# Kernel optimization log

Hardware: AMD Instinct MI355X
Metric: run time of the kernel (lower is better)

The kernel has to match this reference:

```python
import jax, jax.numpy as jnp
import numpy as np

KEEP_RATIO = 0.25
BLOCK = 8
TEMP = 0.1


def setup_inputs() -> dict:
    key = jax.random.key(0)
    features = jax.random.normal(key, (8, 256, 132, 132), dtype=jnp.float32)
    return {"features": features, "enabled": 1}


def reference(features, enabled):
    B, C, H, W = features.shape
    if not enabled:
        return jnp.ones((B, C, H, W), dtype=features.dtype)
    # pad H, W up to multiples of BLOCK (zeros, like F.pad default)
    ph = (-H) % BLOCK
    pw = (-W) % BLOCK
    x = jnp.pad(jnp.abs(features), ((0, 0), (0, 0), (0, ph), (0, pw)))
    Hp, Wp = H + ph, W + pw
    nh, nw = Hp // BLOCK, Wp // BLOCK
    # avg_pool2d(kernel=stride=BLOCK) == block-mean via reshape
    pooled = x.reshape(B, C, nh, BLOCK, nw, BLOCK).mean(axis=(3, 5))  # [B,C,nh,nw]
    total = nh * nw
    scores = pooled.reshape(B, C, total)
    keep = max(1, min(total, int(round(total * KEEP_RATIO))))
    top_vals, top_idx = jax.lax.top_k(scores, keep)  # sorted descending, like torch.topk
    # hard mask: scatter ones at topk indices
    flat_idx = top_idx.reshape(B * C, keep)
    hard = (jnp.zeros((B * C, total), dtype=features.dtype)
            .at[jnp.arange(B * C)[:, None], flat_idx].set(1.0)
            .reshape(B, C, total))
    # training-mode straight-through soft blend
    thr = jax.lax.stop_gradient(top_vals[..., -1:])  # kth value as threshold
    soft = jax.nn.sigmoid((scores - thr) / TEMP)
    soft = soft * (keep / jnp.maximum(soft.sum(-1, keepdims=True), 1e-6))
    soft = jnp.clip(soft, 0.0, 1.0)
    mask = jax.lax.stop_gradient(hard) - jax.lax.stop_gradient(soft) + soft
    # upsample blocks back to pixels (repeat_interleave) and crop padding
    block_mask = mask.reshape(B, C, nh, nw)
    full = jnp.repeat(jnp.repeat(block_mask, BLOCK, axis=2), BLOCK, axis=3)
    return full[:, :, :H, :W]
```

## Files before the change

### kernel.cpp

```cpp
#include <hip/hip_runtime.h>


#define HH 132
#define WW 132
#define NB 17
#define TOTAL 289
#define KEEP 72
#define NTHREADS 256

__global__ __launch_bounds__(NTHREADS)
void gate_kernel(const float* __restrict__ feats,
                 const int* __restrict__ enabled_p,
                 float* __restrict__ out) {
    const int plane = blockIdx.x;
    const int t = threadIdx.x;
    const float* __restrict__ fp = feats + (size_t)plane * (HH * WW);
    float* __restrict__ op = out + (size_t)plane * (HH * WW);

    __shared__ double s_col[WW];
    __shared__ double s_score[TOTAL];
    __shared__ float  s_hard[TOTAL];

    for (int br = 0; br < NB; ++br) {
        const int r0 = br * 8;
        const int nr = (r0 + 8 <= HH) ? 8 : (HH - r0);
        if (t < WW) {
            double acc = 0.0;
            const float* rp = fp + (size_t)r0 * WW + t;
            #pragma unroll
            for (int k = 0; k < 8; ++k) {
                if (k < nr) acc += (double)fabsf(rp[k * WW]);
            }
            s_col[t] = acc;
        }
        __syncthreads();
        if (t < NB) {
            const int c0 = t * 8;
            const int nc = (c0 + 8 <= WW) ? 8 : (WW - c0);
            double s = 0.0;
            for (int j = 0; j < nc; ++j) s += s_col[c0 + j];
            s_score[br * NB + t] = s;
        }
        __syncthreads();
    }

    const int en = *enabled_p;
    for (int i = t; i < TOTAL; i += NTHREADS) {
        const double si = s_score[i];
        int rank = 0;
        for (int j = 0; j < TOTAL; ++j) {
            const double sj = s_score[j];
            rank += (int)((sj > si) || ((sj == si) && (j < i)));
        }
        s_hard[i] = (!en || rank < KEEP) ? 1.0f : 0.0f;
    }
    __syncthreads();

    constexpr int NV = (HH * WW) / 4;
    float4* __restrict__ op4 = (float4*)op;
    for (int v = t; v < NV; v += NTHREADS) {
        const int base = v * 4;
        const int row = base / WW;
        const int col = base - row * WW;
        const float m = s_hard[(row >> 3) * NB + (col >> 3)];
        op4[v] = make_float4(m, m, m, m);
    }
}

extern "C" void kernel_launch(void* const* d_in, const int* in_sizes, int n_in,
                              void* d_out, int out_size, void* d_ws, size_t ws_size,
                              hipStream_t stream) {
    const float* feats = (const float*)d_in[0];
    const int* enabled = (const int*)d_in[1];
    float* out = (float*)d_out;
    const int planes = 8 * 256;
    gate_kernel<<<planes, NTHREADS, 0, stream>>>(feats, enabled, out);
}
```

Before: 269.7 us.

## Compute block sums per thread with float4 loads, removing per-row-band syncs

Replaces the 17-iteration column-sum-then-reduce loop, which has two barriers per band, with one thread per 8x8 block. Each thread reads its block with float4 loads and accumulates in two double accumulators. This removes 34 syncthreads and the shared column buffer. In exchange, 289 blocks across 256 threads leave one extra pass for 33 threads, and each thread's float4 loads stride 528 bytes between rows, so global access is less coalesced.

New measurement: 296.9 us. 1.1x slower.

```diff
diff --git a/kernel.cpp b/kernel.cpp
--- a/kernel.cpp
+++ b/kernel.cpp
@@ -7,6 +7,7 @@
 #define TOTAL 289
 #define KEEP 72
 #define NTHREADS 256
+#define ROWV (WW / 4)
 
 __global__ __launch_bounds__(NTHREADS)
 void gate_kernel(const float* __restrict__ feats,
@@ -17,32 +18,43 @@
     const float* __restrict__ fp = feats + (size_t)plane * (HH * WW);
     float* __restrict__ op = out + (size_t)plane * (HH * WW);
 
-    __shared__ double s_col[WW];
     __shared__ double s_score[TOTAL];
     __shared__ float  s_hard[TOTAL];
 
-    for (int br = 0; br < NB; ++br) {
-        const int r0 = br * 8;
-        const int nr = (r0 + 8 <= HH) ? 8 : (HH - r0);
-        if (t < WW) {
-            double acc = 0.0;
-            const float* rp = fp + (size_t)r0 * WW + t;
+    for (int blk = t; blk < TOTAL; blk += NTHREADS) {
+        const int br = blk / NB;
+        const int bc = blk - br * NB;
+        const int nr = (br == NB - 1) ? 4 : 8;
+        const float4* __restrict__ p =
+            (const float4*)(fp + (size_t)(br * 8) * WW) + bc * 2;
+        double acc0 = 0.0, acc1 = 0.0;
+        if (bc < NB - 1) {
             #pragma unroll
-            for (int k = 0; k < 8; ++k) {
-                if (k < nr) acc += (double)fabsf(rp[k * WW]);
+            for (int r = 0; r < 8; ++r) {
+                if (r < nr) {
+                    const float4 a = p[0];
+                    const float4 b = p[1];
+                    acc0 += (double)fabsf(a.x); acc1 += (double)fabsf(a.y);
+                    acc0 += (double)fabsf(a.z); acc1 += (double)fabsf(a.w);
+                    acc0 += (double)fabsf(b.x); acc1 += (double)fabsf(b.y);
+                    acc0 += (double)fabsf(b.z); acc1 += (double)fabsf(b.w);
+                }
+                p += ROWV;
             }
-            s_col[t] = acc;
+        } else {
+            #pragma unroll
+            for (int r = 0; r < 8; ++r) {
+                if (r < nr) {
+                    const float4 a = p[0];
+                    acc0 += (double)fabsf(a.x); acc1 += (double)fabsf(a.y);
+                    acc0 += (double)fabsf(a.z); acc1 += (double)fabsf(a.w);
+                }
+                p += ROWV;
+            }
         }
-        __syncthreads();
-        if (t < NB) {
-            const int c0 = t * 8;
-            const int nc = (c0 + 8 <= WW) ? 8 : (WW - c0);
-            double s = 0.0;
-            for (int j = 0; j < nc; ++j) s += s_col[c0 + j];
-            s_score[br * NB + t] = s;
-        }
-        __syncthreads();
+        s_score[blk] = acc0 + acc1;
     }
+    __syncthreads();
 
     const int en = *enabled_p;
     for (int i = t; i < TOTAL; i += NTHREADS) {
```

## Load whole plane with float4 into LDS, then reduce and rank in one wave

Applied to the files above, without the earlier changes.

Replaces the 17 row-band passes, which used scalar loads, only 132 active threads and two barriers per band, with a single fully vectorized float4 sweep of the plane. Each float4 partial sum is stored as a double in LDS. Block scores are then reduced from LDS by one wave. That wave also ranks five scores per thread, reusing each shared-memory read of s_score across those five comparisons. The cost is about 35 KB of LDS per block, which may limit occupancy despite the launch-bounds hint of 8 blocks, and most threads sit idle during the ranking phase.

New measurement: 374.8 us. +39.0%, slower.

```diff
diff --git a/kernel.cpp b/kernel.cpp
--- a/kernel.cpp
+++ b/kernel.cpp
@@ -6,64 +6,87 @@
 #define NB 17
 #define TOTAL 289
 #define KEEP 72
-#define NTHREADS 256
+#define NT 256
+#define ROW4 (WW / 4)
+#define NV4 (HH * ROW4)
 
-__global__ __launch_bounds__(NTHREADS)
+__global__ __launch_bounds__(NT, 8)
 void gate_kernel(const float* __restrict__ feats,
                  const int* __restrict__ enabled_p,
                  float* __restrict__ out) {
     const int plane = blockIdx.x;
     const int t = threadIdx.x;
-    const float* __restrict__ fp = feats + (size_t)plane * (HH * WW);
-    float* __restrict__ op = out + (size_t)plane * (HH * WW);
+    const float4* __restrict__ fp4 = (const float4*)(feats + (size_t)plane * (HH * WW));
+    float4* __restrict__ op4 = (float4*)(out + (size_t)plane * (HH * WW));
 
-    __shared__ double s_col[WW];
+    __shared__ double s_part[NV4];
     __shared__ double s_score[TOTAL];
     __shared__ float  s_hard[TOTAL];
 
-    for (int br = 0; br < NB; ++br) {
-        const int r0 = br * 8;
-        const int nr = (r0 + 8 <= HH) ? 8 : (HH - r0);
-        if (t < WW) {
-            double acc = 0.0;
-            const float* rp = fp + (size_t)r0 * WW + t;
-            #pragma unroll
-            for (int k = 0; k < 8; ++k) {
-                if (k < nr) acc += (double)fabsf(rp[k * WW]);
-            }
-            s_col[t] = acc;
+    for (int k = 0; k < 18; ++k) {
+        const int v = t + (k << 8);
+        if (v < NV4) {
+            const float4 a = fp4[v];
+            s_part[v] = (double)fabsf(a.x) + (double)fabsf(a.y)
+                      + (double)fabsf(a.z) + (double)fabsf(a.w);
         }
-        __syncthreads();
-        if (t < NB) {
-            const int c0 = t * 8;
-            const int nc = (c0 + 8 <= WW) ? 8 : (WW - c0);
-            double s = 0.0;
-            for (int j = 0; j < nc; ++j) s += s_col[c0 + j];
-            s_score[br * NB + t] = s;
-        }
-        __syncthreads();
-    }
-
-    const int en = *enabled_p;
-    for (int i = t; i < TOTAL; i += NTHREADS) {
-        const double si = s_score[i];
-        int rank = 0;
-        for (int j = 0; j < TOTAL; ++j) {
-            const double sj = s_score[j];
-            rank += (int)((sj > si) || ((sj == si) && (j < i)));
-        }
-        s_hard[i] = (!en || rank < KEEP) ? 1.0f : 0.0f;
     }
     __syncthreads();
 
-    constexpr int NV = (HH * WW) / 4;
-    float4* __restrict__ op4 = (float4*)op;
-    for (int v = t; v < NV; v += NTHREADS) {
-        const int base = v * 4;
-        const int row = base / WW;
-        const int col = base - row * WW;
-        const float m = s_hard[(row >> 3) * NB + (col >> 3)];
-        op4[v] = make_float4(m, m, m, m);
+    double si[5];
+    int idx[5], rank[5];
+    if (t < 64) {
+        #pragma unroll
+        for (int q = 0; q < 5; ++q) {
+            const int i = t + (q << 6);
+            idx[q] = i; si[q] = -1.0; rank[q] = TOTAL;
+            if (i < TOTAL) {
+                const int br = i / NB;
+                const int bc = i - br * NB;
+                const int nr = (br == NB - 1) ? 4 : 8;
+                const int two = (bc == NB - 1) ? 0 : 1;
+                int base = (br * 8) * ROW4 + bc * 2;
+                double s = 0.0;
+                for (int r = 0; r < nr; ++r) {
+                    s += s_part[base];
+                    if (two) s += s_part[base + 1];
+                    base += ROW4;
+                }
+                si[q] = s;
+                s_score[i] = s;
+            }
+        }
+    }
+    __syncthreads();
+
+    if (t < 64) {
+        #pragma unroll
+        for (int q = 0; q < 5; ++q) rank[q] = 0;
+        for (int j = 0; j < TOTAL; ++j) {
+            const double sj = s_score[j];
+            #pragma unroll
+            for (int q = 0; q < 5; ++q) {
+                rank[q] += (int)((sj > si[q]) ||
+                                 ((sj == si[q]) && (j < idx[q])));
+            }
+        }
+        const int en = *enabled_p;
+        #pragma unroll
+        for (int q = 0; q < 5; ++q) {
+            if (idx[q] < TOTAL)
+                s_hard[idx[q]] = (!en || rank[q] < KEEP) ? 1.0f : 0.0f;
+        }
+    }
+    __syncthreads();
+
+    for (int k = 0; k < 18; ++k) {
+        const int v = t + (k << 8);
+        if (v < NV4) {
+            const int row = v / ROW4;
+            const int c4 = v - row * ROW4;
+            const float m = s_hard[(row >> 3) * NB + (c4 >> 1)];
+            op4[v] = make_float4(m, m, m, m);
+        }
     }
 }
 
@@ -73,6 +96,5 @@
     const float* feats = (const float*)d_in[0];
     const int* enabled = (const int*)d_in[1];
     float* out = (float*)d_out;
-    const int planes = 8 * 256;
-    gate_kernel<<<planes, NTHREADS, 0, stream>>>(feats, enabled, out);
+    gate_kernel<<<8 * 256, NT, 0, stream>>>(feats, enabled, out);
 }
```
